# Optimization experiments

Hardware: AMD Instinct MI355X
Metric: run time of the kernel (lower is better)

The kernel has to match this reference:

```python
import jax, jax.numpy as jnp
import numpy as np

H = 768
R = 24


def setup_inputs() -> dict:
    key = jax.random.key(0)
    ks = jax.random.split(key, 9)
    B, S = 4, 256
    hidden = jax.random.normal(ks[0], (B, S, H), dtype=jnp.float32)
    # ConcatHandshaking fc: Linear(2H -> H); torch weight shape (out,in)=(H,2H)
    fc_w = jax.random.normal(ks[1], (H, 2 * H), dtype=jnp.float32) * (1.0 / np.sqrt(2 * H))
    fc_b = jnp.zeros((H,), dtype=jnp.float32)
    # h2t: Linear(H -> 2)
    h2t_w = jax.random.normal(ks[2], (2, H), dtype=jnp.float32) * (1.0 / np.sqrt(H))
    h2t_b = jnp.zeros((2,), dtype=jnp.float32)
    # h2h / t2t TaggingProjector: R independent Linear(H -> 3), batched as (R,3,H)
    h2h_w = jax.random.normal(ks[3], (R, 3, H), dtype=jnp.float32) * (1.0 / np.sqrt(H))
    h2h_b = jnp.zeros((R, 3), dtype=jnp.float32)
    t2t_w = jax.random.normal(ks[4], (R, 3, H), dtype=jnp.float32) * (1.0 / np.sqrt(H))
    t2t_b = jnp.zeros((R, 3), dtype=jnp.float32)
    return {
        "hidden": hidden,
        "fc_w": fc_w, "fc_b": fc_b,
        "h2t_w": h2t_w, "h2t_b": h2t_b,
        "h2h_w": h2h_w, "h2h_b": h2h_b,
        "t2t_w": t2t_w, "t2t_b": t2t_b,
    }


def _handshaking(hidden, fc_w, fc_b):
    # hidden: (B, S, H). Pairs (i, j) with i <= j in row-major (torch loop) order.
    S = hidden.shape[1]
    idx_i, idx_j = jnp.triu_indices(S)  # each (P,), P = S(S+1)/2
    # concat([h_i, h_j]) @ W^T == h_i @ Wl^T + h_j @ Wr^T  (avoids (B,P,2H) buffer)
    Wl = fc_w[:, :H]  # (H, H)
    Wr = fc_w[:, H:]  # (H, H)
    left = jnp.einsum('bsh,oh->bso', hidden, Wl)   # (B, S, H)
    right = jnp.einsum('bsh,oh->bso', hidden, Wr)  # (B, S, H)
    hs = jnp.tanh(left[:, idx_i, :] + right[:, idx_j, :] + fc_b)  # (B, P, H)
    return hs


def reference(hidden, fc_w, fc_b, h2t_w, h2t_b, h2h_w, h2h_b, t2t_w, t2t_b):
    hs = _handshaking(hidden, fc_w, fc_b)  # (B, P, H)
    # h2t: plain Linear(H->2), logits (no softmax in original)
    h2t = jnp.einsum('bph,oh->bpo', hs, h2t_w) + h2t_b  # (B, P, 2)
    # TaggingProjector: batched per-relation Linear(H->3), then softmax over tags
    h2h = jax.nn.softmax(jnp.einsum('bph,rth->brpt', hs, h2h_w) + h2h_b[None, :, None, :], axis=-1)
    t2t = jax.nn.softmax(jnp.einsum('bph,rth->brpt', hs, t2t_w) + t2t_b[None, :, None, :], axis=-1)
    return (h2t, h2h, t2t)
```

## Files before the change

kernel.cpp:

```cpp
#include <hip/hip_runtime.h>
#include <hip/hip_bf16.h>

#define H 768
#define SEQ 256
#define NPAIR 32896
#define NTOT 131584
#define NOUTP 160
#define OFF_H2H 263168u
#define OFF_T2T 9737216u

#define N_BPK 122880
#define N_FCW 1179648
#define SCL 2.8853900817779268f

#define CH 32
#define NCH 24
#define BSLOT 12288
#define SLAB_STR 166

typedef short bf16x8 __attribute__((ext_vector_type(8)));
typedef float f32x4 __attribute__((ext_vector_type(4)));

__device__ __forceinline__ float tanh_s(float xs) {
    float e = __builtin_amdgcn_exp2f(xs);
    return fmaf(-2.0f, __builtin_amdgcn_rcpf(e + 1.0f), 1.0f);
}
__device__ __forceinline__ float bf_lo(int w){ return __uint_as_float(((unsigned)w) << 16); }
__device__ __forceinline__ float bf_hi(int w){ return __uint_as_float(((unsigned)w) & 0xffff0000u); }
__device__ __forceinline__ float bfu(unsigned short u){ return __uint_as_float(((unsigned)u) << 16); }
__device__ __forceinline__ int cvtpk(float lo, float hi) {
    int r;
    asm("v_cvt_pk_bf16_f32 %0, %1, %2" : "=v"(r) : "v"(lo), "v"(hi));
    return r;
}
__device__ __forceinline__ unsigned short bf16r(float x){
    unsigned int u = __float_as_uint(x);
    u += 0x7fffu + ((u >> 16) & 1u);
    return (unsigned short)(u >> 16);
}
__device__ __forceinline__ bf16x8 tanh_frag(int4 lv, int4 rv) {
    int4 st;
    st.x = cvtpk(tanh_s(bf_lo(lv.x) + bf_lo(rv.x)), tanh_s(bf_hi(lv.x) + bf_hi(rv.x)));
    st.y = cvtpk(tanh_s(bf_lo(lv.y) + bf_lo(rv.y)), tanh_s(bf_hi(lv.y) + bf_hi(rv.y)));
    st.z = cvtpk(tanh_s(bf_lo(lv.z) + bf_lo(rv.z)), tanh_s(bf_hi(lv.z) + bf_hi(rv.z)));
    st.w = cvtpk(tanh_s(bf_lo(lv.w) + bf_lo(rv.w)), tanh_s(bf_hi(lv.w) + bf_hi(rv.w)));
    return __builtin_bit_cast(bf16x8, st);
}

typedef const __attribute__((address_space(1))) unsigned int* as1_u32p;
typedef __attribute__((address_space(3))) unsigned int* as3_u32p;
__device__ __forceinline__ void gload_lds16(const void* g, void* l) {
    __builtin_amdgcn_global_load_lds((as1_u32p)g, (as3_u32p)l, 16, 0, 0);
}

__device__ __forceinline__ int row_start(int i) { return i * SEQ - (i * (i - 1)) / 2; }
__device__ __forceinline__ void pair_ij(int p, int& oi, int& oj) {
    double disc = 263169.0 - 8.0 * (double)p;
    int i = (int)((513.0 - sqrt(disc)) * 0.5);
    if (i > 0 && row_start(i) > p) --i;
    while (row_start(i + 1) <= p) ++i;
    oi = i;
    oj = i + (p - row_start(i));
}
__device__ __forceinline__ int batch_of(int g) {
    return (g >= 3 * NPAIR) ? 3 : (g >= 2 * NPAIR) ? 2 : (g >= NPAIR) ? 1 : 0;
}

__global__ __launch_bounds__(256) void pack_kernel(
    const float* __restrict__ h2t_w, const float* __restrict__ h2h_w,
    const float* __restrict__ t2t_w, const float* __restrict__ h2t_b,
    const float* __restrict__ h2h_b, const float* __restrict__ t2t_b,
    const float* __restrict__ fc_w,
    unsigned short* __restrict__ Bpk, unsigned short* __restrict__ fcwb,
    float* __restrict__ bc)
{
    int idx = blockIdx.x * 256 + threadIdx.x;
    if (idx < N_BPK) {
        int j = idx & 7, lane = (idx >> 3) & 63, rest = idx >> 9;
        int f = rest % 10, c = rest / 10;
        int n = f * 16 + (lane & 15);
        int k = c * CH + ((lane >> 4) << 3) + j;
        float v = 0.f;
        if (n < 2)        v = h2t_w[n * H + k];
        else if (n < 74)  v = h2h_w[(n - 2) * H + k];
        else if (n < 146) v = t2t_w[(n - 74) * H + k];
        Bpk[c * 6144 + (idx - c * 5120)] = bf16r(v);
    } else if (idx < N_BPK + N_FCW) {
        int q = idx - N_BPK;
        int n = q / H, k = q % H;
        float v = (n < H) ? fc_w[(size_t)n * 2 * H + k]
                          : fc_w[(size_t)(n - H) * 2 * H + H + k];
        fcwb[q] = bf16r(v);
    } else if (idx < N_BPK + N_FCW + NOUTP) {
        int q = idx - N_BPK - N_FCW;
        float v = 0.f;
        if (q < 2)        v = h2t_b[q];
        else if (q < 74)  v = h2h_b[q - 2];
        else if (q < 146) v = t2t_b[q - 74];
        bc[q] = v;
    }
}

__global__ __launch_bounds__(256, 2) void lr_mfma(
    const float* __restrict__ hidden, const unsigned short* __restrict__ fcwb,
    const float* __restrict__ fc_b,
    unsigned short* __restrict__ LB, unsigned short* __restrict__ RB)
{
    __shared__ __align__(16) char sm[24576];
    const int tid = threadIdx.x, l = tid & 63, w = tid >> 6;
    const int wm = w >> 1, wn = w & 1;
    const int m0 = blockIdx.x * 64, n0 = blockIdx.y * 128;
    f32x4 acc[2][4] = {};
    for (int c = 0; c < 12; ++c) {
        const int k0 = c * 64;
        #pragma unroll
        for (int it = 0; it < 2; ++it) {
            int idx = tid + it * 256;
            int row = idx >> 3, k8 = idx & 7;
            const float4* src = reinterpret_cast<const float4*>(hidden + (size_t)(m0 + row) * H + k0 + k8 * 8);
            float4 a = src[0], bq = src[1];
            int4 st;
            st.x = cvtpk(a.x, a.y);  st.y = cvtpk(a.z, a.w);
            st.z = cvtpk(bq.x, bq.y); st.w = cvtpk(bq.z, bq.w);
            *reinterpret_cast<int4*>(sm + row * 128 + ((k8 * 16) ^ ((row & 7) << 4))) = st;
        }
        #pragma unroll
        for (int it = 0; it < 4; ++it) {
            int idx = tid + it * 256;
            int row = idx >> 3, k8 = idx & 7;
            *reinterpret_cast<int4*>(sm + 8192 + row * 128 + ((k8 * 16) ^ ((row & 7) << 4))) =
                *reinterpret_cast<const int4*>(fcwb + (size_t)(n0 + row) * H + k0 + k8 * 8);
        }
        __syncthreads();
        #pragma unroll
        for (int kk = 0; kk < 2; ++kk) {
            const int sl = kk * 4 + (l >> 4);
            const int swz = (l & 7) << 4;
            bf16x8 af[2], bfr[4];
            #pragma unroll
            for (int a = 0; a < 2; ++a) {
                int row = 32 * wm + 16 * a + (l & 15);
                af[a] = *reinterpret_cast<const bf16x8*>(sm + row * 128 + ((sl * 16) ^ swz));
            }
            #pragma unroll
            for (int f = 0; f < 4; ++f) {
                int row = 64 * wn + 16 * f + (l & 15);
                bfr[f] = *reinterpret_cast<const bf16x8*>(sm + 8192 + row * 128 + ((sl * 16) ^ swz));
            }
            #pragma unroll
            for (int a = 0; a < 2; ++a)
                #pragma unroll
                for (int f = 0; f < 4; ++f)
                    acc[a][f] = __builtin_amdgcn_mfma_f32_16x16x32_bf16(af[a], bfr[f], acc[a][f], 0, 0, 0);
        }
        __syncthreads();
    }
    #pragma unroll
    for (int a = 0; a < 2; ++a)
        #pragma unroll
        for (int f = 0; f < 4; ++f)
            #pragma unroll
            for (int r = 0; r < 4; ++r) {
                int row = m0 + 32 * wm + 16 * a + 4 * (l >> 4) + r;
                int col = n0 + 64 * wn + 16 * f + (l & 15);
                float v = acc[a][f][r];
                if (n0 < H) LB[(size_t)row * H + col] = bf16r((v + fc_b[col]) * SCL);
                else        RB[(size_t)row * H + (col - H)] = bf16r(v * SCL);
            }
}

__global__ __launch_bounds__(256, 4) void pair_mfma(
    const unsigned short* __restrict__ LB, const unsigned short* __restrict__ RB,
    const unsigned short* __restrict__ Bpk, const float* __restrict__ bc,
    float* __restrict__ out)
{
    __shared__ __align__(16) char sm[25216];
    int*   iOf  = reinterpret_cast<int*>(sm);
    int*   jOf  = reinterpret_cast<int*>(sm + 256);
    float* bc_s = reinterpret_cast<float*>(sm + 24576);

    const int tid = threadIdx.x, l = tid & 63, w = tid >> 6;
    const int g0 = blockIdx.x * 64;
    const int b = batch_of(g0);
    const int p0 = g0 - b * NPAIR;

    if (tid < 64) {
        int i, j; pair_ij(p0 + tid, i, j);
        iOf[tid] = (b * SEQ + i) * H;
        jOf[tid] = (b * SEQ + j) * H;
    }
    if (tid < NOUTP) bc_s[tid] = bc[tid];
    __syncthreads();

    const int row = 16 * w + (l & 15);
    const unsigned short* lp = LB + iOf[row] + ((l >> 4) << 3);
    const unsigned short* rp = RB + jOf[row] + ((l >> 4) << 3);
    __syncthreads();

    const char* bp = reinterpret_cast<const char*>(Bpk) + w * 1024 + l * 16;
    const int d0 = w * 1024;

    f32x4 acc[10] = {};

    {
        gload_lds16(bp,        sm + d0);
        gload_lds16(bp + 4096, sm + 4096 + d0);
        gload_lds16(bp + 8192, sm + 8192 + d0);
        __builtin_amdgcn_sched_barrier(0);
    }
    int4 lvC = *reinterpret_cast<const int4*>(lp);
    int4 rvC = *reinterpret_cast<const int4*>(rp);
    asm volatile("s_waitcnt vmcnt(2)" ::: "memory");
    __builtin_amdgcn_s_barrier();
    __builtin_amdgcn_sched_barrier(0);

    for (int c = 0; c < NCH - 1; ++c) {
        char* bufn = sm + (((c + 1) & 1) ? BSLOT : 0);
        const char* bn = bp + (c + 1) * BSLOT;
        gload_lds16(bn,        bufn + d0);
        gload_lds16(bn + 4096, bufn + 4096 + d0);
        gload_lds16(bn + 8192, bufn + 8192 + d0);
        __builtin_amdgcn_sched_barrier(0);
        bf16x8 a0 = tanh_frag(lvC, rvC);
        const int co = (c + 1) * CH;
        int4 lvN = *reinterpret_cast<const int4*>(lp + co);
        int4 rvN = *reinterpret_cast<const int4*>(rp + co);
        const char* bufc = sm + ((c & 1) ? BSLOT : 0);
        #pragma unroll
        for (int f = 0; f < 10; ++f) {
            bf16x8 bfr = *reinterpret_cast<const bf16x8*>(bufc + (f * 64 + l) * 16);
            acc[f] = __builtin_amdgcn_mfma_f32_16x16x32_bf16(a0, bfr, acc[f], 0, 0, 0);
        }
        asm volatile("s_waitcnt vmcnt(2)" ::: "memory");
        __builtin_amdgcn_s_barrier();
        __builtin_amdgcn_sched_barrier(0);
        lvC = lvN; rvC = rvN;
    }
    {
        bf16x8 a0 = tanh_frag(lvC, rvC);
        const char* bufc = sm + BSLOT;
        #pragma unroll
        for (int f = 0; f < 10; ++f) {
            bf16x8 bfr = *reinterpret_cast<const bf16x8*>(bufc + (f * 64 + l) * 16);
            acc[f] = __builtin_amdgcn_mfma_f32_16x16x32_bf16(a0, bfr, acc[f], 0, 0, 0);
        }
    }
    asm volatile("s_waitcnt lgkmcnt(0)" ::: "memory");
    __builtin_amdgcn_s_barrier();

    unsigned short* slab = reinterpret_cast<unsigned short*>(sm);
    #pragma unroll
    for (int f = 0; f < 10; ++f)
        #pragma unroll
        for (int r = 0; r < 4; ++r) {
            int rw = 16 * w + 4 * (l >> 4) + r;
            slab[rw * SLAB_STR + f * 16 + (l & 15)] = bf16r(acc[f][r]);
        }
    __syncthreads();

    if (tid < 128) {
        int pr = tid >> 1, tt = tid & 1;
        float val = bfu(slab[pr * SLAB_STR + tt]) + bc_s[tt];
        __builtin_nontemporal_store(val, &out[(size_t)(g0 + pr) * 2 + tt]);
    }
    #pragma unroll
    for (int it = 0; it < 12; ++it) {
        int item = it * 256 + tid;
        int pr = item & 63, rr = item >> 6;
        int p = p0 + pr;
        int ob = 2 + rr * 3;
        const unsigned short* sp = slab + pr * SLAB_STR + ob;
        float l0 = bfu(sp[0]) + bc_s[ob + 0];
        float l1 = bfu(sp[1]) + bc_s[ob + 1];
        float l2 = bfu(sp[2]) + bc_s[ob + 2];
        float mx = fmaxf(l0, fmaxf(l1, l2));
        float e0 = __expf(l0 - mx), e1 = __expf(l1 - mx), e2 = __expf(l2 - mx);
        float inv = __fdividef(1.0f, e0 + e1 + e2);
        size_t base = (rr < 24)
            ? (size_t)OFF_H2H + ((size_t)(b * 24 + rr) * NPAIR + p) * 3
            : (size_t)OFF_T2T + ((size_t)(b * 24 + rr - 24) * NPAIR + p) * 3;
        __builtin_nontemporal_store(e0 * inv, &out[base + 0]);
        __builtin_nontemporal_store(e1 * inv, &out[base + 1]);
        __builtin_nontemporal_store(e2 * inv, &out[base + 2]);
    }
}

extern "C" void kernel_launch(void* const* d_in, const int* in_sizes, int n_in,
                              void* d_out, int out_size, void* d_ws, size_t ws_size,
                              hipStream_t stream) {
    const float* hidden = (const float*)d_in[0];
    const float* fc_w   = (const float*)d_in[1];
    const float* fc_b   = (const float*)d_in[2];
    const float* h2t_w  = (const float*)d_in[3];
    const float* h2t_b  = (const float*)d_in[4];
    const float* h2h_w  = (const float*)d_in[5];
    const float* h2h_b  = (const float*)d_in[6];
    const float* t2t_w  = (const float*)d_in[7];
    const float* t2t_b  = (const float*)d_in[8];

    char* wsb = (char*)d_ws;
    unsigned short* LBw  = (unsigned short*)(wsb);
    unsigned short* RBw  = (unsigned short*)(wsb + 1572864);
    unsigned short* Bpk  = (unsigned short*)(wsb + 3145728);
    unsigned short* fcwb = (unsigned short*)(wsb + 3440640);
    float*          bc   = (float*)        (wsb + 5799936);

    float* out = (float*)d_out;

    pack_kernel<<<(N_BPK + N_FCW + NOUTP + 255) / 256, 256, 0, stream>>>(
        h2t_w, h2h_w, t2t_w, h2t_b, h2h_b, t2t_b, fc_w, Bpk, fcwb, bc);
    lr_mfma<<<dim3(16, 12), 256, 0, stream>>>(hidden, fcwb, fc_b, LBw, RBw);
    pair_mfma<<<NTOT / 64, 256, 0, stream>>>(LBw, RBw, Bpk, bc, out);
}
```

Baseline: 95.75 us.

## Enlarge pair-kernel tiles to 128 pairs and K-chunk 64, halve lr_mfma N tile

The pair kernel now processes 128 pairs per 512-thread block, and each pipeline step covers a K chunk of 64 split into two MFMA sub-steps, so there are half as many barrier and double-buffer iterations. Bpk is repacked to match the new chunk layout. The pair indices are computed per lane instead of through an LDS table. Separately, lr_mfma uses 64-wide N tiles on a grid twice as large for more parallelism. In exchange, the pair kernel needs more LDS per block and more registers, which can lower occupancy.

```diff
diff --git a/kernel.cpp b/kernel.cpp
--- a/kernel.cpp
+++ b/kernel.cpp
@@ -13,9 +13,9 @@
 #define N_FCW 1179648
 #define SCL 2.8853900817779268f
 
-#define CH 32
-#define NCH 24
-#define BSLOT 12288
+#define CH 64
+#define NCH 12
+#define BSLOT 24576
 #define SLAB_STR 166
 
 typedef short bf16x8 __attribute__((ext_vector_type(8)));
@@ -77,14 +77,15 @@
     int idx = blockIdx.x * 256 + threadIdx.x;
     if (idx < N_BPK) {
         int j = idx & 7, lane = (idx >> 3) & 63, rest = idx >> 9;
-        int f = rest % 10, c = rest / 10;
+        int frag = rest % 20, c = rest / 20;
+        int f = frag % 10, kk = frag / 10;
         int n = f * 16 + (lane & 15);
-        int k = c * CH + ((lane >> 4) << 3) + j;
+        int k = c * CH + kk * 32 + ((lane >> 4) << 3) + j;
         float v = 0.f;
         if (n < 2)        v = h2t_w[n * H + k];
         else if (n < 74)  v = h2h_w[(n - 2) * H + k];
         else if (n < 146) v = t2t_w[(n - 74) * H + k];
-        Bpk[c * 6144 + (idx - c * 5120)] = bf16r(v);
+        Bpk[c * 12288 + (idx - c * 10240)] = bf16r(v);
     } else if (idx < N_BPK + N_FCW) {
         int q = idx - N_BPK;
         int n = q / H, k = q % H;
@@ -106,11 +107,11 @@
     const float* __restrict__ fc_b,
     unsigned short* __restrict__ LB, unsigned short* __restrict__ RB)
 {
-    __shared__ __align__(16) char sm[24576];
+    __shared__ __align__(16) char sm[16384];
     const int tid = threadIdx.x, l = tid & 63, w = tid >> 6;
     const int wm = w >> 1, wn = w & 1;
-    const int m0 = blockIdx.x * 64, n0 = blockIdx.y * 128;
-    f32x4 acc[2][4] = {};
+    const int m0 = blockIdx.x * 64, n0 = blockIdx.y * 64;
+    f32x4 acc[2][2] = {};
     for (int c = 0; c < 12; ++c) {
         const int k0 = c * 64;
         #pragma unroll
@@ -125,7 +126,7 @@
             *reinterpret_cast<int4*>(sm + row * 128 + ((k8 * 16) ^ ((row & 7) << 4))) = st;
         }
         #pragma unroll
-        for (int it = 0; it < 4; ++it) {
+        for (int it = 0; it < 2; ++it) {
             int idx = tid + it * 256;
             int row = idx >> 3, k8 = idx & 7;
             *reinterpret_cast<int4*>(sm + 8192 + row * 128 + ((k8 * 16) ^ ((row & 7) << 4))) =
@@ -136,21 +137,21 @@
         for (int kk = 0; kk < 2; ++kk) {
             const int sl = kk * 4 + (l >> 4);
             const int swz = (l & 7) << 4;
-            bf16x8 af[2], bfr[4];
+            bf16x8 af[2], bfr[2];
             #pragma unroll
             for (int a = 0; a < 2; ++a) {
                 int row = 32 * wm + 16 * a + (l & 15);
                 af[a] = *reinterpret_cast<const bf16x8*>(sm + row * 128 + ((sl * 16) ^ swz));
             }
             #pragma unroll
-            for (int f = 0; f < 4; ++f) {
-                int row = 64 * wn + 16 * f + (l & 15);
+            for (int f = 0; f < 2; ++f) {
+                int row = 32 * wn + 16 * f + (l & 15);
                 bfr[f] = *reinterpret_cast<const bf16x8*>(sm + 8192 + row * 128 + ((sl * 16) ^ swz));
             }
             #pragma unroll
             for (int a = 0; a < 2; ++a)
                 #pragma unroll
-                for (int f = 0; f < 4; ++f)
+                for (int f = 0; f < 2; ++f)
                     acc[a][f] = __builtin_amdgcn_mfma_f32_16x16x32_bf16(af[a], bfr[f], acc[a][f], 0, 0, 0);
         }
         __syncthreads();
@@ -158,92 +159,103 @@
     #pragma unroll
     for (int a = 0; a < 2; ++a)
         #pragma unroll
-        for (int f = 0; f < 4; ++f)
+        for (int f = 0; f < 2; ++f)
             #pragma unroll
             for (int r = 0; r < 4; ++r) {
                 int row = m0 + 32 * wm + 16 * a + 4 * (l >> 4) + r;
-                int col = n0 + 64 * wn + 16 * f + (l & 15);
+                int col = n0 + 32 * wn + 16 * f + (l & 15);
                 float v = acc[a][f][r];
                 if (n0 < H) LB[(size_t)row * H + col] = bf16r((v + fc_b[col]) * SCL);
                 else        RB[(size_t)row * H + (col - H)] = bf16r(v * SCL);
             }
 }
 
-__global__ __launch_bounds__(256, 4) void pair_mfma(
+__global__ __launch_bounds__(512, 2) void pair_mfma(
     const unsigned short* __restrict__ LB, const unsigned short* __restrict__ RB,
     const unsigned short* __restrict__ Bpk, const float* __restrict__ bc,
     float* __restrict__ out)
 {
-    __shared__ __align__(16) char sm[25216];
-    int*   iOf  = reinterpret_cast<int*>(sm);
-    int*   jOf  = reinterpret_cast<int*>(sm + 256);
-    float* bc_s = reinterpret_cast<float*>(sm + 24576);
+    __shared__ __align__(16) char sm[49792];
+    float* bc_s = reinterpret_cast<float*>(sm + 49152);
 
     const int tid = threadIdx.x, l = tid & 63, w = tid >> 6;
-    const int g0 = blockIdx.x * 64;
+    const int g0 = blockIdx.x * 128;
     const int b = batch_of(g0);
     const int p0 = g0 - b * NPAIR;
 
-    if (tid < 64) {
-        int i, j; pair_ij(p0 + tid, i, j);
-        iOf[tid] = (b * SEQ + i) * H;
-        jOf[tid] = (b * SEQ + j) * H;
-    }
     if (tid < NOUTP) bc_s[tid] = bc[tid];
-    __syncthreads();
 
     const int row = 16 * w + (l & 15);
-    const unsigned short* lp = LB + iOf[row] + ((l >> 4) << 3);
-    const unsigned short* rp = RB + jOf[row] + ((l >> 4) << 3);
-    __syncthreads();
-
-    const char* bp = reinterpret_cast<const char*>(Bpk) + w * 1024 + l * 16;
-    const int d0 = w * 1024;
+    int pi, pj;
+    pair_ij(p0 + row, pi, pj);
+    const int kb = (l >> 4) << 3;
+    const unsigned short* lp = LB + (size_t)(b * SEQ + pi) * H + kb;
+    const unsigned short* rp = RB + (size_t)(b * SEQ + pj) * H + kb;
+
+    const char* bpk = reinterpret_cast<const char*>(Bpk);
+    const int soff = tid * 16;
+    const int doff = w * 1024;
 
     f32x4 acc[10] = {};
 
     {
-        gload_lds16(bp,        sm + d0);
-        gload_lds16(bp + 4096, sm + 4096 + d0);
-        gload_lds16(bp + 8192, sm + 8192 + d0);
+        gload_lds16(bpk + soff,          sm + doff);
+        gload_lds16(bpk + soff + 8192,   sm + doff + 8192);
+        gload_lds16(bpk + soff + 16384,  sm + doff + 16384);
         __builtin_amdgcn_sched_barrier(0);
     }
-    int4 lvC = *reinterpret_cast<const int4*>(lp);
-    int4 rvC = *reinterpret_cast<const int4*>(rp);
-    asm volatile("s_waitcnt vmcnt(2)" ::: "memory");
+    int4 lv0 = *reinterpret_cast<const int4*>(lp);
+    int4 lv1 = *reinterpret_cast<const int4*>(lp + 32);
+    int4 rv0 = *reinterpret_cast<const int4*>(rp);
+    int4 rv1 = *reinterpret_cast<const int4*>(rp + 32);
+    asm volatile("s_waitcnt vmcnt(4) lgkmcnt(0)" ::: "memory");
     __builtin_amdgcn_s_barrier();
     __builtin_amdgcn_sched_barrier(0);
 
+    #pragma unroll 2
     for (int c = 0; c < NCH - 1; ++c) {
         char* bufn = sm + (((c + 1) & 1) ? BSLOT : 0);
-        const char* bn = bp + (c + 1) * BSLOT;
-        gload_lds16(bn,        bufn + d0);
-        gload_lds16(bn + 4096, bufn + 4096 + d0);
-        gload_lds16(bn + 8192, bufn + 8192 + d0);
+        const char* bn = bpk + (c + 1) * BSLOT + soff;
+        gload_lds16(bn,          bufn + doff);
+        gload_lds16(bn + 8192,   bufn + doff + 8192);
+        gload_lds16(bn + 16384,  bufn + doff + 16384);
         __builtin_amdgcn_sched_barrier(0);
-        bf16x8 a0 = tanh_frag(lvC, rvC);
+        bf16x8 a0 = tanh_frag(lv0, rv0);
+        bf16x8 a1 = tanh_frag(lv1, rv1);
         const int co = (c + 1) * CH;
-        int4 lvN = *reinterpret_cast<const int4*>(lp + co);
-        int4 rvN = *reinterpret_cast<const int4*>(rp + co);
+        lv0 = *reinterpret_cast<const int4*>(lp + co);
+        lv1 = *reinterpret_cast<const int4*>(lp + co + 32);
+        rv0 = *reinterpret_cast<const int4*>(rp + co);
+        rv1 = *reinterpret_cast<const int4*>(rp + co + 32);
         const char* bufc = sm + ((c & 1) ? BSLOT : 0);
         #pragma unroll
         for (int f = 0; f < 10; ++f) {
             bf16x8 bfr = *reinterpret_cast<const bf16x8*>(bufc + (f * 64 + l) * 16);
             acc[f] = __builtin_amdgcn_mfma_f32_16x16x32_bf16(a0, bfr, acc[f], 0, 0, 0);
         }
-        asm volatile("s_waitcnt vmcnt(2)" ::: "memory");
+        #pragma unroll
+        for (int f = 0; f < 10; ++f) {
+            bf16x8 bfr = *reinterpret_cast<const bf16x8*>(bufc + ((10 + f) * 64 + l) * 16);
+            acc[f] = __builtin_amdgcn_mfma_f32_16x16x32_bf16(a1, bfr, acc[f], 0, 0, 0);
+        }
+        asm volatile("s_waitcnt vmcnt(4) lgkmcnt(0)" ::: "memory");
         __builtin_amdgcn_s_barrier();
         __builtin_amdgcn_sched_barrier(0);
-        lvC = lvN; rvC = rvN;
     }
     {
-        bf16x8 a0 = tanh_frag(lvC, rvC);
+        bf16x8 a0 = tanh_frag(lv0, rv0);
+        bf16x8 a1 = tanh_frag(lv1, rv1);
         const char* bufc = sm + BSLOT;
         #pragma unroll
         for (int f = 0; f < 10; ++f) {
             bf16x8 bfr = *reinterpret_cast<const bf16x8*>(bufc + (f * 64 + l) * 16);
             acc[f] = __builtin_amdgcn_mfma_f32_16x16x32_bf16(a0, bfr, acc[f], 0, 0, 0);
         }
+        #pragma unroll
+        for (int f = 0; f < 10; ++f) {
+            bf16x8 bfr = *reinterpret_cast<const bf16x8*>(bufc + ((10 + f) * 64 + l) * 16);
+            acc[f] = __builtin_amdgcn_mfma_f32_16x16x32_bf16(a1, bfr, acc[f], 0, 0, 0);
+        }
     }
     asm volatile("s_waitcnt lgkmcnt(0)" ::: "memory");
     __builtin_amdgcn_s_barrier();
@@ -258,15 +270,15 @@
         }
     __syncthreads();
 
-    if (tid < 128) {
+    if (tid < 256) {
         int pr = tid >> 1, tt = tid & 1;
         float val = bfu(slab[pr * SLAB_STR + tt]) + bc_s[tt];
         __builtin_nontemporal_store(val, &out[(size_t)(g0 + pr) * 2 + tt]);
     }
     #pragma unroll
     for (int it = 0; it < 12; ++it) {
-        int item = it * 256 + tid;
-        int pr = item & 63, rr = item >> 6;
+        int item = it * 512 + tid;
+        int pr = item & 127, rr = item >> 7;
         int p = p0 + pr;
         int ob = 2 + rr * 3;
         const unsigned short* sp = slab + pr * SLAB_STR + ob;
@@ -309,6 +321,6 @@
 
     pack_kernel<<<(N_BPK + N_FCW + NOUTP + 255) / 256, 256, 0, stream>>>(
         h2t_w, h2h_w, t2t_w, h2t_b, h2h_b, t2t_b, fc_w, Bpk, fcwb, bc);
-    lr_mfma<<<dim3(16, 12), 256, 0, stream>>>(hidden, fcwb, fc_b, LBw, RBw);
-    pair_mfma<<<NTOT / 64, 256, 0, stream>>>(LBw, RBw, Bpk, bc, out);
-}
+    lr_mfma<<<dim3(16, 24), 256, 0, stream>>>(hidden, fcwb, fc_b, LBw, RBw);
+    pair_mfma<<<NTOT / 128, 512, 0, stream>>>(LBw, RBw, Bpk, bc, out);
+}
```

New measurement: 98.95 us. 3.3% more time.
